# Performance work log

Measured on AMD Instinct MI355X. Metric: run time of the kernel, lower is better.

Reference implementation:

```python
import jax, jax.numpy as jnp
import numpy as np

S, H, D, NL = 3, 64, 12, 2  # scales, hidden, input_dim, layers
B, L = 512, 512
EPS = 1e-5


def _layernorm(x, g, b):
    m = jnp.mean(x, axis=-1, keepdims=True)
    v = jnp.var(x, axis=-1, keepdims=True)
    return (x - m) * jax.lax.rsqrt(v + EPS) * g + b


def _cell(x_t, h, c, gw, gb, mi_w, mi_b, mo_w, mo_b, w1, b1, w2, b2, lag, lab, log, lob):
    # fused 4-gate linear: [B, in+H] @ [in+H, 4H]
    gates = jnp.concatenate([x_t, h], axis=-1) @ gw + gb
    f, i, g, o = jnp.split(gates, 4, axis=-1)
    c_new = jax.nn.sigmoid(f) * c + jax.nn.sigmoid(i) * jnp.tanh(g)
    h_t = jax.nn.sigmoid(o) * jnp.tanh(c_new)
    # MultiheadAttention with seq_len=1: softmax over one key == 1,
    # so attn_out = out_proj(v_proj(h_t)) exactly (q/k contribute nothing).
    v = h_t @ mi_w[:, 2 * H:] + mi_b[2 * H:]
    a = v @ mo_w + mo_b
    a = jax.nn.gelu(a @ w1 + b1, approximate=False) @ w2 + b2
    a = _layernorm(a, lag, lab)
    return _layernorm(a + h, log, lob), c_new


def _run_xlstm(xi, gw0, gb0, gw1, gb1, mi_w, mi_b, mo_w, mo_b,
               w1, b1, w2, b2, lag, lab, log, lob, rw0, rb0, rw1, rb1):
    # xi: [B, L, D] -> outputs [B, L, H]; 2-layer unidirectional xLSTM (eval: dropout=identity)
    Bb = xi.shape[0]
    z = jnp.zeros((Bb, H), xi.dtype)

    def step(carry, x_t):
        h0, c0, h1, c1 = carry
        h0, c0 = _cell(x_t, h0, c0, gw0, gb0, mi_w[0], mi_b[0], mo_w[0], mo_b[0],
                       w1[0], b1[0], w2[0], b2[0], lag[0], lab[0], log[0], lob[0])
        inp = h0 + x_t @ rw0 + rb0
        h1, c1 = _cell(inp, h1, c1, gw1, gb1, mi_w[1], mi_b[1], mo_w[1], mo_b[1],
                       w1[1], b1[1], w2[1], b2[1], lag[1], lab[1], log[1], lob[1])
        out = h1 + inp @ rw1 + rb1
        return (h0, c0, h1, c1), out

    _, ys = jax.lax.scan(step, (z, z, z, z), jnp.swapaxes(xi, 0, 1))
    return jnp.swapaxes(ys, 0, 1)


def _upsample_linear(xi, out_len):
    # F.interpolate(mode='linear', align_corners=False) on [B, Li, D] time axis
    Li = xi.shape[1]
    if Li == out_len:
        return xi
    sc = Li / out_len
    src = jnp.maximum((jnp.arange(out_len, dtype=jnp.float32) + 0.5) * sc - 0.5, 0.0)
    i0 = jnp.clip(jnp.floor(src).astype(jnp.int32), 0, Li - 1)
    i1 = jnp.minimum(i0 + 1, Li - 1)
    w = (src - i0.astype(jnp.float32))[None, :, None]
    return xi[:, i0] * (1.0 - w) + xi[:, i1] * w


def _forward(x, gw0, gb0, gw1, gb1, mi_w, mi_b, mo_w, mo_b, w1, b1, w2, b2,
             lag, lab, log, lob, rw0, rb0, rw1, rb1, attn_w):
    Ls = x.shape[1]
    ups = []
    for i in (1, 2, 3):
        start = Ls - Ls // i
        ups.append(_upsample_linear(x[:, start:, :], Ls))
    # bug-faithful ordering from source: xlstm[i] consumes upsampled_outputs[i-1]
    xs = jnp.stack([ups[2], ups[0], ups[1]], axis=0)  # [S, B, L, D]
    outs = jax.vmap(_run_xlstm)(xs, gw0, gb0, gw1, gb1, mi_w, mi_b, mo_w, mo_b,
                                w1, b1, w2, b2, lag, lab, log, lob,
                                rw0, rb0, rw1, rb1)      # [S, B, L, H]
    merged = jnp.moveaxis(outs, 0, 1)                    # [B, S, L, H]
    weights = jax.nn.softmax(merged @ attn_w, axis=1)    # softmax over scale dim
    return jnp.sum(merged * weights[..., None], axis=1)  # [B, L, H]


def setup_inputs() -> dict:
    key = jax.random.key(0)
    ks = iter(jax.random.split(key, 32))
    w = lambda *sh: jax.random.normal(next(ks), sh, jnp.float32) * 0.02
    IN0, IN1 = D + H, 2 * H
    return {
        'x': jax.random.normal(next(ks), (B, L, D), jnp.float32),
        'gw0': w(S, IN0, 4 * H), 'gb0': jnp.zeros((S, 4 * H)),
        'gw1': w(S, IN1, 4 * H), 'gb1': jnp.zeros((S, 4 * H)),
        'mi_w': w(S, NL, H, 3 * H), 'mi_b': jnp.zeros((S, NL, 3 * H)),
        'mo_w': w(S, NL, H, H), 'mo_b': jnp.zeros((S, NL, H)),
        'w1': w(S, NL, H, 2 * H), 'b1': jnp.zeros((S, NL, 2 * H)),
        'w2': w(S, NL, 2 * H, H), 'b2': jnp.zeros((S, NL, H)),
        'lag': jnp.ones((S, NL, H)), 'lab': jnp.zeros((S, NL, H)),
        'log': jnp.ones((S, NL, H)), 'lob': jnp.zeros((S, NL, H)),
        'rw0': w(S, D, H), 'rb0': jnp.zeros((S, H)),
        'rw1': w(S, H, H), 'rb1': jnp.zeros((S, H)),
        'attn_w': w(H),
    }


def reference(x, gw0, gb0, gw1, gb1, mi_w, mi_b, mo_w, mo_b, w1, b1, w2, b2,
              lag, lab, log, lob, rw0, rb0, rw1, rb1, attn_w):
    return _forward(x, gw0, gb0, gw1, gb1, mi_w, mi_b, mo_w, mo_b, w1, b1, w2, b2,
                    lag, lab, log, lob, rw0, rb0, rw1, rb1, attn_w)
```

## Files before the change

kernel.cpp:

```cpp
#include <hip/hip_runtime.h>
#include <hip/hip_bf16.h>
#include <math.h>

#define Sn 3
#define Hn 64
#define Dn 12
#define Bn 512
#define Ln 512
#define BC 4
#define IN0 76
#define NIN 22
#define CT 32
#define NCHUNK (Ln / CT)
#define P2OFF 0
#define P1OFF 384
#define GROFF 768
#define CBOFF 1026
#define MEGABLK 1538

#define NINP ((size_t)3 * Bn * CT * 64)
#define NG1R ((size_t)3 * Bn * CT * 320)
#define NMERG ((size_t)3 * Bn * CT * 64)

using bf16 = __hip_bfloat16;
typedef _Float16 h2 __attribute__((ext_vector_type(2)));
typedef _Float16 h4 __attribute__((ext_vector_type(4)));
typedef _Float16 h8t __attribute__((ext_vector_type(8)));
typedef int i2v __attribute__((ext_vector_type(2)));

__device__ __forceinline__ float u2f(unsigned short x) {
    return __uint_as_float(((unsigned int)x) << 16);
}
__device__ __forceinline__ unsigned short f2u(float f) {
    bf16 h = __float2bfloat16(f);
    unsigned short u;
    __builtin_memcpy(&u, &h, 2);
    return u;
}

__device__ __forceinline__ float ex2(float x) {
#if __has_builtin(__builtin_amdgcn_exp2f)
    return __builtin_amdgcn_exp2f(x);
#else
    return exp2f(x);
#endif
}
__device__ __forceinline__ float frcp(float x) {
#if __has_builtin(__builtin_amdgcn_rcpf)
    return __builtin_amdgcn_rcpf(x);
#else
    return 1.0f / x;
#endif
}
__device__ __forceinline__ float sigm(float x) {
    return frcp(1.0f + ex2(-1.44269504f * x));
}
__device__ __forceinline__ float tanhfast(float x) {
    return 1.0f - 2.0f * frcp(1.0f + ex2(2.88539008f * x));
}
__device__ __forceinline__ float gelu_ex(float x) { return 0.5f * x * (1.0f + erff(x * 0.70710678118654752f)); }

__device__ __forceinline__ float fdot2f(h2 a, h2 b, float c) {
#if __has_builtin(__builtin_amdgcn_fdot2)
    return __builtin_amdgcn_fdot2(a, b, c, false);
#else
    return fmaf((float)a.x, (float)b.x, fmaf((float)a.y, (float)b.y, c));
#endif
}
__device__ __forceinline__ h2 cvt2(float x, float y) {
    h2 r; r.x = (_Float16)x; r.y = (_Float16)y; return r;
}
__device__ __forceinline__ h2 mk2(_Float16 a, _Float16 b) {
    h2 r; r.x = a; r.y = b; return r;
}
__device__ __forceinline__ void unpack8(h8t v, h2* out) {
    out[0] = __builtin_shufflevector(v, v, 0, 1);
    out[1] = __builtin_shufflevector(v, v, 2, 3);
    out[2] = __builtin_shufflevector(v, v, 4, 5);
    out[3] = __builtin_shufflevector(v, v, 6, 7);
}

template <int CTRL>
__device__ __forceinline__ float qp(float v) {
    return __int_as_float(__builtin_amdgcn_update_dpp(0, __float_as_int(v), CTRL, 0xF, 0xF, true));
}
__device__ __forceinline__ float qsum(float v) {
    v += qp<0xB1>(v);
    v += qp<0x4E>(v);
    return v;
}
__device__ __forceinline__ float osum(float v) {
    v = qsum(v);
    v += qp<0x141>(v);
    return v;
}
__device__ __forceinline__ float xadd16(float v) {
#if __has_builtin(__builtin_amdgcn_permlane16_swap)
    i2v r = __builtin_amdgcn_permlane16_swap(__float_as_int(v), __float_as_int(v), false, false);
    return __int_as_float(r.x) + __int_as_float(r.y);
#else
    return v + __int_as_float(__builtin_amdgcn_ds_swizzle(__float_as_int(v), 0x401F));
#endif
}
__device__ __forceinline__ float xadd32(float v) {
#if __has_builtin(__builtin_amdgcn_permlane32_swap)
    i2v r = __builtin_amdgcn_permlane32_swap(__float_as_int(v), __float_as_int(v), false, false);
    return __int_as_float(r.x) + __int_as_float(r.y);
#else
    return v + __shfl_xor(v, 32, 64);
#endif
}
__device__ __forceinline__ float redsum64(float v) {
    v += qp<0xB1>(v);
    v += qp<0x4E>(v);
    v += qp<0x141>(v);
    v += qp<0x140>(v);
    v = xadd16(v);
    v = xadd32(v);
    return v;
}

struct ConvArgs {
    const void* src[NIN];
    unsigned dstOff[NIN];
    unsigned n[NIN];
    unsigned blockStart[NIN + 1];
};

__global__ __launch_bounds__(256) void convert_kernel(ConvArgs a, float* __restrict__ dst) {
    __shared__ int sh[4];
    int tid = threadIdx.x;
    const unsigned short* xr = (const unsigned short*)a.src[0];
    int cnt = 0;
    for (int ii = tid; ii < 2048; ii += 256) {
        unsigned e = (xr[ii] >> 7) & 0xFF;
        if (e >= 110 && e <= 133) cnt++;
    }
    for (int o = 32; o > 0; o >>= 1) cnt += __shfl_xor(cnt, o, 64);
    if ((tid & 63) == 0) sh[tid >> 6] = cnt;
    __syncthreads();
    bool isf32 = (sh[0] + sh[1] + sh[2] + sh[3]) < 1640;

    int bid = blockIdx.x;
    int i = 0;
    while (i < NIN - 1 && bid >= (int)a.blockStart[i + 1]) i++;
    unsigned lb = (unsigned)bid - a.blockStart[i];
    unsigned base = lb * 2048 + tid;
    unsigned n = a.n[i];
    float* d = dst + a.dstOff[i];
    const float* sf = (const float*)a.src[i];
    const unsigned short* su = (const unsigned short*)a.src[i];
#pragma unroll
    for (int e = 0; e < 8; e++) {
        unsigned idx = base + e * 256;
        if (idx < n) d[idx] = isf32 ? sf[idx] : u2f(su[idx]);
    }
}

__global__ __launch_bounds__(256) void setup_kernel(
    const unsigned short* __restrict__ xr, int* __restrict__ flag,
    const float* __restrict__ mi_w, const float* __restrict__ mi_b,
    const float* __restrict__ mo_w, const float* __restrict__ mo_b,
    const float* __restrict__ w1, const float* __restrict__ b1,
    float* __restrict__ M1out, float* __restrict__ bias1out,
    const float* __restrict__ gw1, const float* __restrict__ gb1,
    const float* __restrict__ rw1,
    h2* __restrict__ gw1p16, float* __restrict__ gb1p,
    h2* __restrict__ rw1p16) {
    int bid = blockIdx.x;
    int tid = threadIdx.x;
    if (bid < 6) {
        int sl = bid;
        __shared__ float T[64][64];
        __shared__ float bT[64];
        const float* Mv = mi_w + sl * 64 * 192;
        const float* Mo = mo_w + sl * 64 * 64;
        for (int idx = tid; idx < 64 * 64; idx += 256) {
            int k = idx >> 6, n = idx & 63;
            float acc = 0.f;
            for (int j = 0; j < 64; j++) acc += Mv[k * 192 + 128 + j] * Mo[j * 64 + n];
            T[k][n] = acc;
        }
        for (int n = tid; n < 64; n += 256) {
            float acc = mo_b[sl * 64 + n];
            for (int j = 0; j < 64; j++) acc += mi_b[sl * 192 + 128 + j] * Mo[j * 64 + n];
            bT[n] = acc;
        }
        __syncthreads();
        const float* W1 = w1 + sl * 64 * 128;
        for (int idx = tid; idx < 64 * 128; idx += 256) {
            int k = idx >> 7, m = idx & 127;
            float acc = 0.f;
            for (int n = 0; n < 64; n++) acc += T[k][n] * W1[n * 128 + m];
            M1out[sl * 64 * 128 + idx] = acc;
        }
        for (int m = tid; m < 128; m += 256) {
            float acc = b1[sl * 128 + m];
            for (int n = 0; n < 64; n++) acc += bT[n] * W1[n * 128 + m];
            bias1out[sl * 128 + m] = acc;
        }
    } else if (bid < 9) {
        int s = bid - 6;
        const float* G = gw1 + (size_t)s * 128 * 256;
        for (int idx = tid; idx < 32 * 256; idx += 256) {
            int k2 = idx >> 8, p = idx & 255;
            int c = (p & 3) * 64 + ((p >> 6) << 4) + ((p >> 2) & 15);
            gw1p16[((size_t)s * 32 + k2) * 256 + p] =
                cvt2(G[(2 * k2) * 256 + c], G[(2 * k2 + 1) * 256 + c]);
        }
        for (int p = tid; p < 256; p += 256) {
            int c = (p & 3) * 64 + ((p >> 6) << 4) + ((p >> 2) & 15);
            gb1p[s * 256 + p] = gb1[s * 256 + c];
        }
        const float* R = rw1 + (size_t)s * 64 * 64;
        for (int idx = tid; idx < 32 * 64; idx += 256) {
            int k2 = idx >> 6, c = idx & 63;
            rw1p16[((size_t)s * 32 + k2) * 64 + c] =
                cvt2(R[(2 * k2) * 64 + c], R[(2 * k2 + 1) * 64 + c]);
        }
    } else {
        __shared__ int sh[4];
        int cnt = 0;
        for (int ii = tid; ii < 2048; ii += 256) {
            unsigned e = (xr[ii] >> 7) & 0xFF;
            if (e >= 110 && e <= 133) cnt++;
        }
        for (int o = 32; o > 0; o >>= 1) cnt += __shfl_xor(cnt, o, 64);
        if ((tid & 63) == 0) sh[tid >> 6] = cnt;
        __syncthreads();
        if (tid == 0) {
            int tot = sh[0] + sh[1] + sh[2] + sh[3];
            *flag = (tot < 1640) ? 1 : 0;
        }
    }
}

__device__ __forceinline__ void pass1_body(
    int bid,
    const float* __restrict__ x, const float* __restrict__ gw0,
    const float* __restrict__ gb0,
    const float* __restrict__ M1g, const float* __restrict__ bias1g,
    const float* __restrict__ w2g, const float* __restrict__ b2g,
    const float* __restrict__ lag, const float* __restrict__ lab,
    const float* __restrict__ log_, const float* __restrict__ lob,
    const float* __restrict__ rw0, const float* __restrict__ rb0,
    float* __restrict__ gstate, _Float16* __restrict__ inp_w, int t0) {
    const int tid = threadIdx.x;
    const int sIdx = bid >> 7;
    const int gbase = (bid & 127) * BC;
    const int W = tid >> 6, lane = tid & 63;
    const int q = lane >> 2, ks = lane & 3;
    const int oct = lane >> 3, ks8 = lane & 7;
    const int j = W * 16 + q;
    const int cM = W * 32 + q * 2;
    const int uD = W * 16 + oct * 2;

    const int Li = (sIdx == 0) ? 170 : (sIdx == 1 ? 512 : 256);
    const int st = (sIdx == 0) ? 342 : (sIdx == 1 ? 0 : 256);
    const float sc = (float)Li / 512.0f;

    __shared__ float s_x[2][BC][12];
    __shared__ __align__(16) _Float16 s_h16[BC][72];
    __shared__ __align__(16) _Float16 s_ht16[BC][72];
    __shared__ __align__(16) _Float16 s_z16[BC][136];
    __shared__ float s_t2[BC][64];
    __shared__ float s_rw0[768];

    __builtin_amdgcn_s_setprio(1);

    const float* gw0s = gw0 + sIdx * IN0 * 256;
    float wx[12];
    h2 wg16[4][8], wm16[2][8], ww16[2][8];
#pragma unroll
    for (int g = 0; g < 4; g++)
#pragma unroll
        for (int d = 0; d < 3; d++) wx[g * 3 + d] = gw0s[(ks * 3 + d) * 256 + j + 64 * g];
#pragma unroll
    for (int g = 0; g < 4; g++)
#pragma unroll
        for (int kk = 0; kk < 8; kk++)
            wg16[g][kk] = cvt2(gw0s[(12 + ks * 16 + 2 * kk) * 256 + j + 64 * g],
                               gw0s[(12 + ks * 16 + 2 * kk + 1) * 256 + j + 64 * g]);
    const float* M1s = M1g + (sIdx * 2 + 0) * 8192;
#pragma unroll
    for (int cc = 0; cc < 2; cc++)
#pragma unroll
        for (int kk = 0; kk < 8; kk++)
            wm16[cc][kk] = cvt2(M1s[(ks * 16 + 2 * kk) * 128 + cM + cc],
                                M1s[(ks * 16 + 2 * kk + 1) * 128 + cM + cc]);
    const float* w2s = w2g + (sIdx * 2 + 0) * 8192;
#pragma unroll
    for (int cc = 0; cc < 2; cc++)
#pragma unroll
        for (int kk = 0; kk < 8; kk++)
            ww16[cc][kk] = cvt2(w2s[(ks8 * 16 + 2 * kk) * 64 + uD + cc],
                                w2s[(ks8 * 16 + 2 * kk + 1) * 64 + uD + cc]);

    float h_gb[4];
#pragma unroll
    for (int g = 0; g < 4; g++) h_gb[g] = gb0[sIdx * 256 + j + 64 * g];
    float h_b1[2] = {bias1g[(sIdx * 2 + 0) * 128 + cM], bias1g[(sIdx * 2 + 0) * 128 + cM + 1]};
    float h_b2[2] = {b2g[(sIdx * 2 + 0) * 64 + uD], b2g[(sIdx * 2 + 0) * 64 + uD + 1]};
    int ei = (sIdx * 2 + 0) * 64 + lane;
    float eLag = lag[ei], eLab = lab[ei], eLog = log_[ei], eLob = lob[ei];
    float eRb0 = rb0[sIdx * 64 + lane];

    for (int i = tid; i < 768; i += 256) s_rw0[i] = rw0[sIdx * 768 + i];
    {
        int b = tid >> 6, jj = tid & 63;
        float hv = (t0 == 0) ? 0.f : gstate[((size_t)(sIdx * Bn + gbase + b)) * 256 + jj];
        s_h16[b][jj] = (_Float16)hv;
    }
    float cS = (t0 == 0) ? 0.f
                         : gstate[((size_t)(sIdx * Bn + gbase + ks)) * 256 + 64 + j];
    if (tid < BC * 12) {
        int b = tid / 12, d = tid % 12;
        float srcp = fmaxf((t0 + 0.5f) * sc - 0.5f, 0.f);
        int i0 = (int)floorf(srcp); if (i0 > Li - 1) i0 = Li - 1;
        int i1 = i0 + 1; if (i1 > Li - 1) i1 = Li - 1;
        float w = srcp - (float)i0;
        int gb = gbase + b;
        s_x[0][b][d] = x[(gb * Ln + st + i0) * 12 + d] * (1.0f - w) + x[(gb * Ln + st + i1) * 12 + d] * w;
    }
    __syncthreads();

    for (int tt = 0; tt < CT; tt++) {
        const int sl = tt & 1;
        float myF = 0, myI = 0, myG = 0, myO = 0;
#pragma unroll
        for (int b = 0; b < BC; b++) {
            const h8t* hp = (const h8t*)&s_h16[b][ks * 16];
            h8t hv0 = hp[0], hv1 = hp[1];
            h2 hk[8];
            unpack8(hv0, hk); unpack8(hv1, hk + 4);
            float x0 = s_x[sl][b][ks * 3], x1 = s_x[sl][b][ks * 3 + 1], x2 = s_x[sl][b][ks * 3 + 2];
            float acc[4];
#pragma unroll
            for (int g = 0; g < 4; g++) {
                float s0 = (ks == 0) ? h_gb[g] : 0.f;
                acc[g] = fmaf(wx[g * 3], x0, fmaf(wx[g * 3 + 1], x1, fmaf(wx[g * 3 + 2], x2, s0)));
            }
#pragma unroll
            for (int kk = 0; kk < 8; kk++) {
#pragma unroll
                for (int g = 0; g < 4; g++)
                    acc[g] = fdot2f(wg16[g][kk], hk[kk], acc[g]);
            }
            float a0 = qsum(acc[0]);
            float a1 = qsum(acc[1]);
            float a2 = qsum(acc[2]);
            float a3 = qsum(acc[3]);
            if (ks == b) { myF = a0; myI = a1; myG = a2; myO = a3; }
        }
        {
            float cn = sigm(myF) * cS + sigm(myI) * tanhfast(myG);
            cS = cn;
            s_ht16[ks][j] = (_Float16)(sigm(myO) * tanhfast(cn));
        }
        __syncthreads();
        float z0 = 0, z1 = 0;
#pragma unroll
        for (int b = 0; b < BC; b++) {
            const h8t* hp = (const h8t*)&s_ht16[b][ks * 16];
            h8t hv0 = hp[0], hv1 = hp[1];
            h2 hk[8];
            unpack8(hv0, hk); unpack8(hv1, hk + 4);
            float acc0 = (ks == 0) ? h_b1[0] : 0.f;
            float acc1 = (ks == 0) ? h_b1[1] : 0.f;
#pragma unroll
            for (int kk = 0; kk < 8; kk++) {
                acc0 = fdot2f(wm16[0][kk], hk[kk], acc0);
                acc1 = fdot2f(wm16[1][kk], hk[kk], acc1);
            }
            float a0 = qsum(acc0);
            float a1 = qsum(acc1);
            if (ks == b) { z0 = a0; z1 = a1; }
        }
        *(h2*)&s_z16[ks][cM] = cvt2(gelu_ex(z0), gelu_ex(z1));
        __syncthreads();
#pragma unroll
        for (int b = 0; b < BC; b++) {
            const h8t* zp = (const h8t*)&s_z16[b][ks8 * 16];
            h8t zv0 = zp[0], zv1 = zp[1];
            h2 zk[8];
            unpack8(zv0, zk); unpack8(zv1, zk + 4);
            float acc0 = (ks8 == 0) ? h_b2[0] : 0.f;
            float acc1 = (ks8 == 0) ? h_b2[1] : 0.f;
#pragma unroll
            for (int kk = 0; kk < 8; kk++) {
                acc0 = fdot2f(ww16[0][kk], zk[kk], acc0);
                acc1 = fdot2f(ww16[1][kk], zk[kk], acc1);
            }
            float a0 = osum(acc0);
            float a1 = osum(acc1);
            if (ks8 == b) { s_t2[b][uD] = a0; s_t2[b][uD + 1] = a1; }
        }
        __syncthreads();
        {
            const int bb = W;
            float v = s_t2[bb][lane];
            float m = redsum64(v) * (1.0f / 64.0f);
            float var = redsum64(v * v) * (1.0f / 64.0f) - m * m;
            float rs = rsqrtf(fmaxf(var, 0.0f) + 1e-5f);
            float a = (v - m) * rs * eLag + eLab;
            float hOld = (float)s_h16[bb][lane];
            float y = a + hOld;
            float m2 = redsum64(y) * (1.0f / 64.0f);
            float var2 = redsum64(y * y) * (1.0f / 64.0f) - m2 * m2;
            float rs2 = rsqrtf(fmaxf(var2, 0.0f) + 1e-5f);
            float h0n = (y - m2) * rs2 * eLog + eLob;
            s_h16[bb][lane] = (_Float16)h0n;
            float p = h0n + eRb0;
#pragma unroll
            for (int d = 0; d < 12; d++)
                p = fmaf(s_x[sl][bb][d], s_rw0[d * 64 + lane], p);
            inp_w[(((size_t)(sIdx * Bn + gbase + bb)) * CT + tt) * 64 + lane] = (_Float16)p;
            if (tt + 1 < CT && lane < 12) {
                int d = lane;
                int t = t0 + tt + 1;
                float srcp = fmaxf((t + 0.5f) * sc - 0.5f, 0.f);
                int i0 = (int)floorf(srcp); if (i0 > Li - 1) i0 = Li - 1;
                int i1 = i0 + 1; if (i1 > Li - 1) i1 = Li - 1;
                float w = srcp - (float)i0;
                int gb = gbase + bb;
                s_x[sl ^ 1][bb][d] = x[(gb * Ln + st + i0) * 12 + d] * (1.0f - w) +
                                     x[(gb * Ln + st + i1) * 12 + d] * w;
            }
        }
        __syncthreads();
    }
    {
        int b = tid >> 6, jj = tid & 63;
        gstate[((size_t)(sIdx * Bn + gbase + b)) * 256 + jj] = (float)s_h16[b][jj];
    }
    gstate[((size_t)(sIdx * Bn + gbase + ks)) * 256 + 64 + j] = cS;
}

__device__ __forceinline__ void pass2_body(
    int bid,
    const float* __restrict__ gw1,
    const float* __restrict__ M1g, const float* __restrict__ bias1g,
    const float* __restrict__ w2g, const float* __restrict__ b2g,
    const float* __restrict__ lag, const float* __restrict__ lab,
    const float* __restrict__ log_, const float* __restrict__ lob,
    const _Float16* __restrict__ G1Rr, float* __restrict__ gstate,
    unsigned short* __restrict__ merged_w, int t0) {
    const int tid = threadIdx.x;
    const int sIdx = bid >> 7;
    const int gbase = (bid & 127) * BC;
    const int W = tid >> 6, lane = tid & 63;
    const int q = lane >> 2, ks = lane & 3;
    const int oct = lane >> 3, ks8 = lane & 7;
    const int j = W * 16 + q;
    const int cM = W * 32 + q * 2;
    const int uD = W * 16 + oct * 2;

    __shared__ __align__(16) _Float16 p2_h16[BC][72];
    __shared__ __align__(16) _Float16 p2_ht16[BC][72];
    __shared__ __align__(16) _Float16 p2_z16[BC][136];
    __shared__ float p2_t2[BC][64];

    __builtin_amdgcn_s_setprio(1);

    const float* gw1s = gw1 + (size_t)sIdx * 128 * 256;
    h2 wg16[4][8], wm16[2][8], ww16[2][8];
#pragma unroll
    for (int g = 0; g < 4; g++)
#pragma unroll
        for (int kk = 0; kk < 8; kk++)
            wg16[g][kk] = cvt2(gw1s[(64 + ks * 16 + 2 * kk) * 256 + j + 64 * g],
                               gw1s[(64 + ks * 16 + 2 * kk + 1) * 256 + j + 64 * g]);
    const float* M1s = M1g + (sIdx * 2 + 1) * 8192;
#pragma unroll
    for (int cc = 0; cc < 2; cc++)
#pragma unroll
        for (int kk = 0; kk < 8; kk++)
            wm16[cc][kk] = cvt2(M1s[(ks * 16 + 2 * kk) * 128 + cM + cc],
                                M1s[(ks * 16 + 2 * kk + 1) * 128 + cM + cc]);
    const float* w2s = w2g + (sIdx * 2 + 1) * 8192;
#pragma unroll
    for (int cc = 0; cc < 2; cc++)
#pragma unroll
        for (int kk = 0; kk < 8; kk++)
            ww16[cc][kk] = cvt2(w2s[(ks8 * 16 + 2 * kk) * 64 + uD + cc],
                                w2s[(ks8 * 16 + 2 * kk + 1) * 64 + uD + cc]);

    float h_b1[2] = {bias1g[(sIdx * 2 + 1) * 128 + cM], bias1g[(sIdx * 2 + 1) * 128 + cM + 1]};
    float h_b2[2] = {b2g[(sIdx * 2 + 1) * 64 + uD], b2g[(sIdx * 2 + 1) * 64 + uD + 1]};
    int ei = (sIdx * 2 + 1) * 64 + lane;
    float eLag = lag[ei], eLab = lab[ei], eLog = log_[ei], eLob = lob[ei];

    {
        int b = tid >> 6, jj = tid & 63;
        float hv = (t0 == 0) ? 0.f : gstate[((size_t)(sIdx * Bn + gbase + b)) * 256 + 128 + jj];
        p2_h16[b][jj] = (_Float16)hv;
    }
    float cS = (t0 == 0) ? 0.f
                         : gstate[((size_t)(sIdx * Bn + gbase + ks)) * 256 + 192 + j];
    __syncthreads();

    const size_t rowBase = ((size_t)(sIdx * Bn + gbase)) * CT;
    const int pOff = W * 64 + lane;

    float g1rv[BC], rv;
#pragma unroll
    for (int b = 0; b < BC; b++)
        g1rv[b] = (float)G1Rr[(rowBase + (size_t)b * CT) * 320 + pOff];
    rv = (float)G1Rr[(rowBase + (size_t)W * CT) * 320 + 256 + lane];

    for (int tt = 0; tt < CT; tt++) {
        float myF = 0, myI = 0, myG = 0, myO = 0;
#pragma unroll
        for (int b = 0; b < BC; b++) {
            const h8t* hp = (const h8t*)&p2_h16[b][ks * 16];
            h8t hv0 = hp[0], hv1 = hp[1];
            h2 hk[8];
            unpack8(hv0, hk); unpack8(hv1, hk + 4);
            float acc[4];
#pragma unroll
            for (int g = 0; g < 4; g++) acc[g] = (ks == g) ? g1rv[b] : 0.f;
#pragma unroll
            for (int kk = 0; kk < 8; kk++) {
#pragma unroll
                for (int g = 0; g < 4; g++)
                    acc[g] = fdot2f(wg16[g][kk], hk[kk], acc[g]);
            }
            float a0 = qsum(acc[0]);
            float a1 = qsum(acc[1]);
            float a2 = qsum(acc[2]);
            float a3 = qsum(acc[3]);
            if (ks == b) { myF = a0; myI = a1; myG = a2; myO = a3; }
        }
        {
            float cn = sigm(myF) * cS + sigm(myI) * tanhfast(myG);
            cS = cn;
            p2_ht16[ks][j] = (_Float16)(sigm(myO) * tanhfast(cn));
        }
        float g1rn[BC], rn;
        if (tt + 1 < CT) {
#pragma unroll
            for (int b = 0; b < BC; b++)
                g1rn[b] = (float)G1Rr[(rowBase + (size_t)b * CT + tt + 1) * 320 + pOff];
            rn = (float)G1Rr[(rowBase + (size_t)W * CT + tt + 1) * 320 + 256 + lane];
        } else {
#pragma unroll
            for (int b = 0; b < BC; b++) g1rn[b] = 0.f;
            rn = 0.f;
        }
        __syncthreads();
        float z0 = 0, z1 = 0;
#pragma unroll
        for (int b = 0; b < BC; b++) {
            const h8t* hp = (const h8t*)&p2_ht16[b][ks * 16];
            h8t hv0 = hp[0], hv1 = hp[1];
            h2 hk[8];
            unpack8(hv0, hk); unpack8(hv1, hk + 4);
            float acc0 = (ks == 0) ? h_b1[0] : 0.f;
            float acc1 = (ks == 0) ? h_b1[1] : 0.f;
#pragma unroll
            for (int kk = 0; kk < 8; kk++) {
                acc0 = fdot2f(wm16[0][kk], hk[kk], acc0);
                acc1 = fdot2f(wm16[1][kk], hk[kk], acc1);
            }
            float a0 = qsum(acc0);
            float a1 = qsum(acc1);
            if (ks == b) { z0 = a0; z1 = a1; }
        }
        *(h2*)&p2_z16[ks][cM] = cvt2(gelu_ex(z0), gelu_ex(z1));
        __syncthreads();
#pragma unroll
        for (int b = 0; b < BC; b++) {
            const h8t* zp = (const h8t*)&p2_z16[b][ks8 * 16];
            h8t zv0 = zp[0], zv1 = zp[1];
            h2 zk[8];
            unpack8(zv0, zk); unpack8(zv1, zk + 4);
            float acc0 = (ks8 == 0) ? h_b2[0] : 0.f;
            float acc1 = (ks8 == 0) ? h_b2[1] : 0.f;
#pragma unroll
            for (int kk = 0; kk < 8; kk++) {
                acc0 = fdot2f(ww16[0][kk], zk[kk], acc0);
                acc1 = fdot2f(ww16[1][kk], zk[kk], acc1);
            }
            float a0 = osum(acc0);
            float a1 = osum(acc1);
            if (ks8 == b) { p2_t2[b][uD] = a0; p2_t2[b][uD + 1] = a1; }
        }
        __syncthreads();
        {
            const int bb = W;
            float v = p2_t2[bb][lane];
            float m = redsum64(v) * (1.0f / 64.0f);
            float var = redsum64(v * v) * (1.0f / 64.0f) - m * m;
            float rs = rsqrtf(fmaxf(var, 0.0f) + 1e-5f);
            float a = (v - m) * rs * eLag + eLab;
            float hOld = (float)p2_h16[bb][lane];
            float y = a + hOld;
            float m2 = redsum64(y) * (1.0f / 64.0f);
            float var2 = redsum64(y * y) * (1.0f / 64.0f) - m2 * m2;
            float rs2 = rsqrtf(fmaxf(var2, 0.0f) + 1e-5f);
            float h1n = (y - m2) * rs2 * eLog + eLob;
            p2_h16[bb][lane] = (_Float16)h1n;
            merged_w[(((size_t)(sIdx * Bn + gbase + bb)) * CT + tt) * 64 + lane] = f2u(h1n + rv);
        }
        __syncthreads();
#pragma unroll
        for (int b = 0; b < BC; b++) g1rv[b] = g1rn[b];
        rv = rn;
    }
    {
        int b = tid >> 6, jj = tid & 63;
        gstate[((size_t)(sIdx * Bn + gbase + b)) * 256 + 128 + jj] = (float)p2_h16[b][jj];
    }
    gstate[((size_t)(sIdx * Bn + gbase + ks)) * 256 + 192 + j] = cS;
}

__device__ __forceinline__ void g1r_body(
    int bid,
    const h2* __restrict__ gw1p16, const float* __restrict__ gb1p,
    const h2* __restrict__ rw1p16, const float* __restrict__ rb1,
    const _Float16* __restrict__ inp_r, _Float16* __restrict__ G1Rw) {
    const int tid = threadIdx.x;
    const int s = bid / 86;
    const int bb = bid % 86;
    __shared__ __align__(16) h2 s_in2[32][36];

    const int c4 = tid & 63, rg = tid >> 6;
    float4 bias = *(const float4*)(gb1p + s * 256 + c4 * 4);
    float rbias = rb1[s * 64 + c4];
    const h2* Wg = gw1p16 + (size_t)s * 32 * 256;
    const h2* Wr = rw1p16 + (size_t)s * 32 * 64;

    const size_t sRow = (size_t)s * Bn * CT;
    for (int tile = 0; tile < 6; tile++) {
        int tIdx = bb * 6 + tile;
        if (tIdx >= 512) break;
        int r0 = tIdx * 32;
        __syncthreads();
        for (int i = tid; i < 512; i += 256) {
            int r = i >> 4, kq = i & 15;
            h4 v = *(const h4*)(inp_r + (sRow + r0 + r) * 64 + kq * 4);
            s_in2[kq * 2 + 0][r] = mk2(v.x, v.y);
            s_in2[kq * 2 + 1][r] = mk2(v.z, v.w);
        }
        __syncthreads();
        float acc[8][4], accR[8];
#pragma unroll
        for (int r = 0; r < 8; r++) {
            acc[r][0] = bias.x; acc[r][1] = bias.y; acc[r][2] = bias.z; acc[r][3] = bias.w;
            accR[r] = rbias;
        }
#pragma unroll 4
        for (int k2 = 0; k2 < 32; k2++) {
            h8t wv = *(const h8t*)(Wg + (size_t)k2 * 256 + c4 * 4);
            h2 wp[4]; unpack8(wv, wp);
            h2 wR = Wr[k2 * 64 + c4];
            const h8t* ip = (const h8t*)&s_in2[k2][rg * 8];
            h8t iv0 = ip[0], iv1 = ip[1];
            h2 in2[8]; unpack8(iv0, in2); unpack8(iv1, in2 + 4);
#pragma unroll
            for (int r = 0; r < 8; r++) {
                acc[r][0] = fdot2f(in2[r], wp[0], acc[r][0]);
                acc[r][1] = fdot2f(in2[r], wp[1], acc[r][1]);
                acc[r][2] = fdot2f(in2[r], wp[2], acc[r][2]);
                acc[r][3] = fdot2f(in2[r], wp[3], acc[r][3]);
                accR[r] = fdot2f(in2[r], wR, accR[r]);
            }
        }
#pragma unroll
        for (int r = 0; r < 8; r++) {
            size_t row = sRow + r0 + rg * 8 + r;
            h4 o;
            o.x = (_Float16)acc[r][0]; o.y = (_Float16)acc[r][1];
            o.z = (_Float16)acc[r][2]; o.w = (_Float16)acc[r][3];
            *(h4*)(G1Rw + row * 320 + c4 * 4) = o;
            G1Rw[row * 320 + 256 + c4] = (_Float16)accR[r];
        }
    }
}

__device__ __forceinline__ void combine_body(
    int bid,
    const unsigned short* __restrict__ merged_r,
    const float* __restrict__ attn_w,
    void* __restrict__ outv, const int* __restrict__ flag, int t0) {
    int W = threadIdx.x >> 6, lane = threadIdx.x & 63;
    float aw = attn_w[lane];
    size_t stride = (size_t)Bn * CT * 64;
    int isf = *flag;
#pragma unroll
    for (int r = 0; r < 8; r++) {
        int wid = (bid * 4 + W) * 8 + r;
        int b = wid >> 5, tt = wid & 31;
        size_t base = (((size_t)b) * CT + tt) * 64 + lane;
        float m0 = u2f(merged_r[base]);
        float m1 = u2f(merged_r[base + stride]);
        float m2 = u2f(merged_r[base + 2 * stride]);
        float e0 = redsum64(m0 * aw);
        float e1 = redsum64(m1 * aw);
        float e2 = redsum64(m2 * aw);
        float mx = fmaxf(e0, fmaxf(e1, e2));
        float x0 = expf(e0 - mx), x1 = expf(e1 - mx), x2 = expf(e2 - mx);
        float inv = 1.0f / (x0 + x1 + x2);
        float val = (x0 * m0 + x1 * m1 + x2 * m2) * inv;
        size_t ob = (((size_t)b) * Ln + t0 + tt) * 64 + lane;
        if (isf) ((float*)outv)[ob] = val;
        else ((unsigned short*)outv)[ob] = f2u(val);
    }
}

__global__ __launch_bounds__(256) __attribute__((amdgpu_waves_per_eu(2, 5)))
void mega_kernel(
    const float* __restrict__ x, const float* __restrict__ gw0,
    const float* __restrict__ gb0, const float* __restrict__ gw1,
    const h2* __restrict__ gw1p16, const float* __restrict__ gb1p,
    const h2* __restrict__ rw1p16,
    const float* __restrict__ M1g, const float* __restrict__ bias1g,
    const float* __restrict__ w2g, const float* __restrict__ b2g,
    const float* __restrict__ lag, const float* __restrict__ lab,
    const float* __restrict__ log_, const float* __restrict__ lob,
    const float* __restrict__ rw0, const float* __restrict__ rb0,
    const float* __restrict__ rb1,
    float* __restrict__ gstate,
    _Float16* __restrict__ inpB, _Float16* __restrict__ G1RB,
    unsigned short* __restrict__ mergedB,
    const float* __restrict__ attn_w, void* __restrict__ outv,
    const int* __restrict__ flag,
    int c_p1, int c_g1r, int c_p2, int c_comb) {
    int bid = blockIdx.x;
    if (bid < P1OFF) {
        if (c_p2 >= 0) {
            const _Float16* g1r_r = G1RB + (size_t)(c_p2 & 1) * NG1R;
            unsigned short* merged_w = mergedB + (size_t)(c_p2 & 1) * NMERG;
            pass2_body(bid, gw1, M1g, bias1g, w2g, b2g, lag, lab, log_, lob,
                       g1r_r, gstate, merged_w, c_p2 * CT);
        }
    } else if (bid < GROFF) {
        if (c_p1 >= 0) {
            _Float16* inp_w = inpB + (size_t)(c_p1 & 1) * NINP;
            pass1_body(bid - P1OFF, x, gw0, gb0, M1g, bias1g, w2g, b2g,
                       lag, lab, log_, lob, rw0, rb0, gstate, inp_w, c_p1 * CT);
        }
    } else if (bid < CBOFF) {
        if (c_g1r >= 0) {
            const _Float16* inp_r = inpB + (size_t)(c_g1r & 1) * NINP;
            _Float16* g1r_w = G1RB + (size_t)(c_g1r & 1) * NG1R;
            g1r_body(bid - GROFF, gw1p16, gb1p, rw1p16, rb1, inp_r, g1r_w);
        }
    } else {
        if (c_comb >= 0) {
            const unsigned short* merged_r = mergedB + (size_t)(c_comb & 1) * NMERG;
            combine_body(bid - CBOFF, merged_r, attn_w, outv, flag, c_comb * CT);
        }
    }
}

extern "C" void kernel_launch(void* const* d_in, const int* in_sizes, int n_in,
                              void* d_out, int out_size, void* d_ws, size_t ws_size,
                              hipStream_t stream) {
    (void)out_size; (void)ws_size;
    int* flag = (int*)d_ws;
    float* canon = (float*)((char*)d_ws + 16);

    ConvArgs ca;
    size_t tot = 0;
    unsigned nblocks = 0;
    for (int i = 0; i < NIN; i++) {
        ca.src[i] = d_in[i];
        ca.dstOff[i] = (unsigned)tot;
        unsigned n = (unsigned)in_sizes[i];
        ca.n[i] = n;
        ca.blockStart[i] = nblocks;
        nblocks += (n + 2047) / 2048;
        tot += n;
    }
    ca.blockStart[NIN] = nblocks;

    size_t canonBytes = (tot * 4 + 15) & ~(size_t)15;
    char* p = (char*)d_ws + 16 + canonBytes;
    float* M1 = (float*)p;       p += (size_t)3 * 2 * 64 * 128 * 4;
    float* bias1 = (float*)p;    p += (size_t)3 * 2 * 128 * 4;
    float* gb1p = (float*)p;     p += (size_t)3 * 256 * 4;
    h2* gw1p16 = (h2*)p;         p += (size_t)3 * 32 * 256 * 4;
    h2* rw1p16 = (h2*)p;         p += (size_t)3 * 32 * 64 * 4;
    float* gstate = (float*)p;   p += (size_t)3 * 512 * 256 * 4;
    p = (char*)(((uintptr_t)p + 15) & ~(uintptr_t)15);
    _Float16* inpB = (_Float16*)p;      p += 2 * NINP * 2;
    _Float16* G1RB = (_Float16*)p;      p += 2 * NG1R * 2;
    p = (char*)(((uintptr_t)p + 15) & ~(uintptr_t)15);
    unsigned short* mergedB = (unsigned short*)p;

    const float* x    = canon + ca.dstOff[0];
    const float* gw0  = canon + ca.dstOff[1];
    const float* gb0  = canon + ca.dstOff[2];
    const float* gw1  = canon + ca.dstOff[3];
    const float* gb1  = canon + ca.dstOff[4];
    const float* mi_w = canon + ca.dstOff[5];
    const float* mi_b = canon + ca.dstOff[6];
    const float* mo_w = canon + ca.dstOff[7];
    const float* mo_b = canon + ca.dstOff[8];
    const float* w1   = canon + ca.dstOff[9];
    const float* b1   = canon + ca.dstOff[10];
    const float* w2   = canon + ca.dstOff[11];
    const float* b2   = canon + ca.dstOff[12];
    const float* lag  = canon + ca.dstOff[13];
    const float* lab  = canon + ca.dstOff[14];
    const float* log_ = canon + ca.dstOff[15];
    const float* lob  = canon + ca.dstOff[16];
    const float* rw0  = canon + ca.dstOff[17];
    const float* rb0  = canon + ca.dstOff[18];
    const float* rw1  = canon + ca.dstOff[19];
    const float* rb1  = canon + ca.dstOff[20];
    const float* attn_w = canon + ca.dstOff[21];

    convert_kernel<<<dim3(nblocks), dim3(256), 0, stream>>>(ca, canon);
    setup_kernel<<<dim3(10), dim3(256), 0, stream>>>(
        (const unsigned short*)d_in[0], flag,
        mi_w, mi_b, mo_w, mo_b, w1, b1, M1, bias1,
        gw1, gb1, rw1, gw1p16, gb1p, rw1p16);

    for (int m = 0; m <= NCHUNK + 2; m++) {
        int c1 = (m < NCHUNK) ? m : -1;
        int cg = (m - 1 >= 0 && m - 1 < NCHUNK) ? m - 1 : -1;
        int c2 = (m - 2 >= 0 && m - 2 < NCHUNK) ? m - 2 : -1;
        int cc = (m - 3 >= 0 && m - 3 < NCHUNK) ? m - 3 : -1;
        mega_kernel<<<dim3(MEGABLK), dim3(256), 0, stream>>>(
            x, gw0, gb0, gw1, gw1p16, gb1p, rw1p16, M1, bias1, w2, b2,
            lag, lab, log_, lob, rw0, rb0, rb1, gstate, inpB, G1RB, mergedB,
            attn_w, d_out, flag, c1, cg, c2, cc);
    }
}
```

Before: 3.038 ms.

## Stage per-step outputs in shared memory and prefetch next-step loads earlier

Pass1 and pass2 no longer write per-timestep fp16 outputs straight to global memory. They collect them in a shared scratch buffer and write the whole chunk out at the end with 16-byte vector stores. Pass1 also issues the global loads of the next interpolated x row at the start of each step, and pass2 moves its next-step G1R loads before the gate computation, so the latency overlaps with compute. The cost is an extra 16KB of shared memory per block, which may reduce occupancy.

```diff
diff --git a/kernel.cpp b/kernel.cpp
--- a/kernel.cpp
+++ b/kernel.cpp
@@ -244,7 +244,8 @@
     const float* __restrict__ lag, const float* __restrict__ lab,
     const float* __restrict__ log_, const float* __restrict__ lob,
     const float* __restrict__ rw0, const float* __restrict__ rb0,
-    float* __restrict__ gstate, _Float16* __restrict__ inp_w, int t0) {
+    float* __restrict__ gstate, _Float16* __restrict__ inp_w,
+    _Float16* __restrict__ s_buf, int t0) {
     const int tid = threadIdx.x;
     const int sIdx = bid >> 7;
     const int gbase = (bid & 127) * BC;
@@ -326,6 +327,17 @@
 
     for (int tt = 0; tt < CT; tt++) {
         const int sl = tt & 1;
+        float px0 = 0.f, px1 = 0.f, pw = 0.f;
+        if (tt + 1 < CT && lane < 12) {
+            int t = t0 + tt + 1;
+            float srcp = fmaxf((t + 0.5f) * sc - 0.5f, 0.f);
+            int i0 = (int)floorf(srcp); if (i0 > Li - 1) i0 = Li - 1;
+            int i1 = i0 + 1; if (i1 > Li - 1) i1 = Li - 1;
+            pw = srcp - (float)i0;
+            int gb = gbase + W;
+            px0 = x[(gb * Ln + st + i0) * 12 + lane];
+            px1 = x[(gb * Ln + st + i1) * 12 + lane];
+        }
         float myF = 0, myI = 0, myG = 0, myO = 0;
 #pragma unroll
         for (int b = 0; b < BC; b++) {
@@ -414,18 +426,9 @@
 #pragma unroll
             for (int d = 0; d < 12; d++)
                 p = fmaf(s_x[sl][bb][d], s_rw0[d * 64 + lane], p);
-            inp_w[(((size_t)(sIdx * Bn + gbase + bb)) * CT + tt) * 64 + lane] = (_Float16)p;
-            if (tt + 1 < CT && lane < 12) {
-                int d = lane;
-                int t = t0 + tt + 1;
-                float srcp = fmaxf((t + 0.5f) * sc - 0.5f, 0.f);
-                int i0 = (int)floorf(srcp); if (i0 > Li - 1) i0 = Li - 1;
-                int i1 = i0 + 1; if (i1 > Li - 1) i1 = Li - 1;
-                float w = srcp - (float)i0;
-                int gb = gbase + bb;
-                s_x[sl ^ 1][bb][d] = x[(gb * Ln + st + i0) * 12 + d] * (1.0f - w) +
-                                     x[(gb * Ln + st + i1) * 12 + d] * w;
-            }
+            s_buf[((size_t)bb * CT + tt) * 64 + lane] = (_Float16)p;
+            if (tt + 1 < CT && lane < 12)
+                s_x[sl ^ 1][W][lane] = px0 * (1.0f - pw) + px1 * pw;
         }
         __syncthreads();
     }
@@ -434,6 +437,15 @@
         gstate[((size_t)(sIdx * Bn + gbase + b)) * 256 + jj] = (float)s_h16[b][jj];
     }
     gstate[((size_t)(sIdx * Bn + gbase + ks)) * 256 + 64 + j] = cS;
+
+    {
+        const size_t rowBase = ((size_t)(sIdx * Bn + gbase)) * CT;
+        const h8t* srcp = (const h8t*)s_buf;
+        h8t* dstp = (h8t*)(inp_w + rowBase * 64);
+#pragma unroll
+        for (int i = 0; i < 4; i++)
+            dstp[tid + i * 256] = srcp[tid + i * 256];
+    }
 }
 
 __device__ __forceinline__ void pass2_body(
@@ -444,7 +456,8 @@
     const float* __restrict__ lag, const float* __restrict__ lab,
     const float* __restrict__ log_, const float* __restrict__ lob,
     const _Float16* __restrict__ G1Rr, float* __restrict__ gstate,
-    unsigned short* __restrict__ merged_w, int t0) {
+    unsigned short* __restrict__ merged_w,
+    _Float16* __restrict__ s_buf, int t0) {
     const int tid = threadIdx.x;
     const int sIdx = bid >> 7;
     const int gbase = (bid & 127) * BC;
@@ -501,6 +514,7 @@
 
     const size_t rowBase = ((size_t)(sIdx * Bn + gbase)) * CT;
     const int pOff = W * 64 + lane;
+    unsigned short* s_mrg = (unsigned short*)s_buf;
 
     float g1rv[BC], rv;
 #pragma unroll
@@ -509,6 +523,17 @@
     rv = (float)G1Rr[(rowBase + (size_t)W * CT) * 320 + 256 + lane];
 
     for (int tt = 0; tt < CT; tt++) {
+        float g1rn[BC], rn;
+        if (tt + 1 < CT) {
+#pragma unroll
+            for (int b = 0; b < BC; b++)
+                g1rn[b] = (float)G1Rr[(rowBase + (size_t)b * CT + tt + 1) * 320 + pOff];
+            rn = (float)G1Rr[(rowBase + (size_t)W * CT + tt + 1) * 320 + 256 + lane];
+        } else {
+#pragma unroll
+            for (int b = 0; b < BC; b++) g1rn[b] = 0.f;
+            rn = 0.f;
+        }
         float myF = 0, myI = 0, myG = 0, myO = 0;
 #pragma unroll
         for (int b = 0; b < BC; b++) {
@@ -535,17 +560,6 @@
             float cn = sigm(myF) * cS + sigm(myI) * tanhfast(myG);
             cS = cn;
             p2_ht16[ks][j] = (_Float16)(sigm(myO) * tanhfast(cn));
-        }
-        float g1rn[BC], rn;
-        if (tt + 1 < CT) {
-#pragma unroll
-            for (int b = 0; b < BC; b++)
-                g1rn[b] = (float)G1Rr[(rowBase + (size_t)b * CT + tt + 1) * 320 + pOff];
-            rn = (float)G1Rr[(rowBase + (size_t)W * CT + tt + 1) * 320 + 256 + lane];
-        } else {
-#pragma unroll
-            for (int b = 0; b < BC; b++) g1rn[b] = 0.f;
-            rn = 0.f;
         }
         __syncthreads();
         float z0 = 0, z1 = 0;
@@ -600,7 +614,7 @@
             float rs2 = rsqrtf(fmaxf(var2, 0.0f) + 1e-5f);
             float h1n = (y - m2) * rs2 * eLog + eLob;
             p2_h16[bb][lane] = (_Float16)h1n;
-            merged_w[(((size_t)(sIdx * Bn + gbase + bb)) * CT + tt) * 64 + lane] = f2u(h1n + rv);
+            s_mrg[((size_t)bb * CT + tt) * 64 + lane] = f2u(h1n + rv);
         }
         __syncthreads();
 #pragma unroll
@@ -612,6 +626,14 @@
         gstate[((size_t)(sIdx * Bn + gbase + b)) * 256 + 128 + jj] = (float)p2_h16[b][jj];
     }
     gstate[((size_t)(sIdx * Bn + gbase + ks)) * 256 + 192 + j] = cS;
+
+    {
+        const h8t* srcp = (const h8t*)s_mrg;
+        h8t* dstp = (h8t*)(merged_w + rowBase * 64);
+#pragma unroll
+        for (int i = 0; i < 4; i++)
+            dstp[tid + i * 256] = srcp[tid + i * 256];
+    }
 }
 
 __device__ __forceinline__ void g1r_body(
@@ -726,19 +748,21 @@
     const float* __restrict__ attn_w, void* __restrict__ outv,
     const int* __restrict__ flag,
     int c_p1, int c_g1r, int c_p2, int c_comb) {
+    __shared__ __align__(16) _Float16 s_scratch[(size_t)BC * CT * 64];
     int bid = blockIdx.x;
     if (bid < P1OFF) {
         if (c_p2 >= 0) {
             const _Float16* g1r_r = G1RB + (size_t)(c_p2 & 1) * NG1R;
             unsigned short* merged_w = mergedB + (size_t)(c_p2 & 1) * NMERG;
             pass2_body(bid, gw1, M1g, bias1g, w2g, b2g, lag, lab, log_, lob,
-                       g1r_r, gstate, merged_w, c_p2 * CT);
+                       g1r_r, gstate, merged_w, s_scratch, c_p2 * CT);
         }
     } else if (bid < GROFF) {
         if (c_p1 >= 0) {
             _Float16* inp_w = inpB + (size_t)(c_p1 & 1) * NINP;
             pass1_body(bid - P1OFF, x, gw0, gb0, M1g, bias1g, w2g, b2g,
-                       lag, lab, log_, lob, rw0, rb0, gstate, inp_w, c_p1 * CT);
+                       lag, lab, log_, lob, rw0, rb0, gstate, inp_w,
+                       s_scratch, c_p1 * CT);
         }
     } else if (bid < CBOFF) {
         if (c_g1r >= 0) {
```

Result: no change. 3.075 ms (+1.2%).
